# Performance work log

Measured on AMD Instinct MI355X. Metric: run time of the kernel, lower is better.

The kernel has to match this reference:

```python
import jax, jax.numpy as jnp
import numpy as np

HIDDEN = 128
GRID = 8
NB = 32.0            # neighborhood_size
CELL = NB / GRID      # cell_size


def setup_inputs() -> dict:
    key = jax.random.key(0)
    k1, k2, k3, k4 = jax.random.split(key, 4)
    N = 1024
    hidden_states = jax.random.normal(k1, (N, HIDDEN), dtype=jnp.float32)
    positions = jax.random.uniform(k2, (N, 2), dtype=jnp.float32) * 100.0
    fan_in = GRID * GRID * HIDDEN
    bound = 1.0 / np.sqrt(fan_in)
    W = jax.random.uniform(k3, (fan_in, HIDDEN), dtype=jnp.float32, minval=-bound, maxval=bound)
    b = jax.random.uniform(k4, (HIDDEN,), dtype=jnp.float32, minval=-bound, maxval=bound)
    return {"hidden_states": hidden_states, "positions": positions, "W": W, "b": b}


def reference(hidden_states, positions, W, b):
    N, H = hidden_states.shape
    G = GRID
    pos = jax.lax.stop_gradient(positions)  # indices carry no gradient (matches torch int())
    # rel[i, j] = positions[j] - positions[i]
    rel = pos[None, :, :] - pos[:, None, :]                      # [N, N, 2]
    half = NB / 2.0
    inside = (jnp.abs(rel[..., 0]) <= half) & (jnp.abs(rel[..., 1]) <= half)
    not_self = ~jnp.eye(N, dtype=bool)
    valid = inside & not_self                                     # [N, N]
    # rel + half is in [0, NB] when inside, so floor == int() truncation
    gx = jnp.clip(jnp.floor((rel[..., 0] + half) / CELL).astype(jnp.int32), 0, G - 1)
    gy = jnp.clip(jnp.floor((rel[..., 1] + half) / CELL).astype(jnp.int32), 0, G - 1)
    cell = gy * G + gx                                            # [N, N], in [0, G*G)
    # invalid pairs go to a dummy cell G*G per pedestrian
    seg = jnp.where(valid, cell, G * G)
    gid = (jnp.arange(N, dtype=jnp.int32)[:, None] * (G * G + 1) + seg).reshape(-1)
    data = jnp.broadcast_to(hidden_states[None, :, :], (N, N, H)).reshape(N * N, H)
    gmax = jax.ops.segment_max(data, gid, num_segments=N * (G * G + 1))  # [N*(G*G+1), H]
    # torch grid starts at zeros and uses maximum -> clamp at 0; empty cells (-inf) -> 0
    grid = jnp.maximum(gmax.reshape(N, G * G + 1, H)[:, : G * G, :], 0.0)  # [N, G*G, H]
    flat = grid.reshape(N, G * G * H)
    return flat @ W + b
```

## Files before the change

### kernel.cpp

```cpp
#include <hip/hip_runtime.h>
#include <hip/hip_bf16.h>

#define N_PED 1024
#define H 128
#define G 8
#define NCELL 64
#define K_TOT 8192
#define HALF_NB 16.0f
#define INV_CELL 0.25f

#define KSPLIT 16
#define KC 512
#define BM 32
#define BK 64
#define NSTAGE 8

typedef __attribute__((ext_vector_type(8))) short bf16x8;
typedef __attribute__((ext_vector_type(4))) float f32x4;

__device__ __forceinline__ unsigned map_f2u(float v) {
    unsigned u = __float_as_uint(v);
    return (u & 0x80000000u) ? ~u : (u | 0x80000000u);
}
__device__ __forceinline__ float unmap_u2f(unsigned u) {
    return __uint_as_float((u & 0x80000000u) ? (u ^ 0x80000000u) : ~u);
}
__device__ __forceinline__ ushort f2bf(float f) {
    unsigned u = __float_as_uint(f);
    return (ushort)((u + 0x7FFFu + ((u >> 16) & 1u)) >> 16);
}
__device__ __forceinline__ void gl_lds16(const void* g, void* l) {
    __builtin_amdgcn_global_load_lds(
        (const __attribute__((address_space(1))) void*)g,
        (__attribute__((address_space(3))) void*)l, 16, 0, 0);
}

__global__ __launch_bounds__(512) void fused_pre(const float* __restrict__ hs,
                                                 const float* __restrict__ pos,
                                                 const float* __restrict__ W,
                                                 ushort* __restrict__ grid,
                                                 ushort* __restrict__ Wt) {
    __shared__ __align__(16) char smem[36872];
    const int tid = threadIdx.x;

    if (blockIdx.x < N_PED) {
        unsigned* lgrid = (unsigned*)smem;
        int*      list  = (int*)(smem + 32768);
        int*      cnt   = (int*)(smem + 36864);
        const int i = blockIdx.x;

        const unsigned iu = 0x80000000u;
        uint4 iv = {iu, iu, iu, iu};
        for (int k = tid; k < NCELL * H / 4; k += 512) ((uint4*)lgrid)[k] = iv;
        if (tid == 0) *cnt = 0;
        __syncthreads();

        const float2 pi = ((const float2*)pos)[i];
        for (int j = tid; j < N_PED; j += 512) {
            float2 pj = ((const float2*)pos)[j];
            float rx = pj.x - pi.x;
            float ry = pj.y - pi.y;
            if (j != i && fabsf(rx) <= HALF_NB && fabsf(ry) <= HALF_NB) {
                int gx = (int)floorf((rx + HALF_NB) * INV_CELL);
                int gy = (int)floorf((ry + HALF_NB) * INV_CELL);
                gx = min(G - 1, max(0, gx));
                gy = min(G - 1, max(0, gy));
                int slot = atomicAdd(cnt, 1);
                list[slot] = (j << 8) | (gy * G + gx);
            }
        }
        __syncthreads();

        const int n    = *cnt;
        const int dim4 = (tid & 31) * 4;
        const int eg   = tid >> 5;
        int e  = eg;
        int p0 = (e < n) ? list[e] : -1;
        int p1 = (e + 16 < n) ? list[e + 16] : -1;
        float4 v0 = {};
        if (p0 >= 0) v0 = *(const float4*)&hs[(p0 >> 8) * H + dim4];
        while (p0 >= 0) {
            int p2 = (e + 32 < n) ? list[e + 32] : -1;
            float4 v1 = {};
            if (p1 >= 0) v1 = *(const float4*)&hs[(p1 >> 8) * H + dim4];
            unsigned* gph = &lgrid[(p0 & 255) * H + dim4];
            atomicMax(gph + 0, map_f2u(v0.x));
            atomicMax(gph + 1, map_f2u(v0.y));
            atomicMax(gph + 2, map_f2u(v0.z));
            atomicMax(gph + 3, map_f2u(v0.w));
            e += 16; p0 = p1; p1 = p2; v0 = v1;
        }
        __syncthreads();

        ushort* dst = grid + (size_t)i * K_TOT;
        for (int c = tid; c < K_TOT / 8; c += 512) {
            uint4 a = ((const uint4*)lgrid)[2 * c];
            uint4 b = ((const uint4*)lgrid)[2 * c + 1];
            ushort tmp[8];
            tmp[0] = f2bf(unmap_u2f(a.x)); tmp[1] = f2bf(unmap_u2f(a.y));
            tmp[2] = f2bf(unmap_u2f(a.z)); tmp[3] = f2bf(unmap_u2f(a.w));
            tmp[4] = f2bf(unmap_u2f(b.x)); tmp[5] = f2bf(unmap_u2f(b.y));
            tmp[6] = f2bf(unmap_u2f(b.z)); tmp[7] = f2bf(unmap_u2f(b.w));
            *(bf16x8*)&dst[8 * c] = *(const bf16x8*)tmp;
        }
    } else {
        float* tile = (float*)smem;
        const int bw  = blockIdx.x - N_PED;
        const int k0w = bw * 64;

        for (int x = tid; x < 64 * H; x += 512) {
            int r = x >> 7, c = x & 127;
            tile[r * 129 + c] = W[(size_t)(k0w + r) * H + c];
        }
        __syncthreads();

        const int col = tid >> 2;
        const int kh  = (tid & 3) * 16;
        ushort tmp[16];
        #pragma unroll
        for (int t = 0; t < 16; ++t) tmp[t] = f2bf(tile[(kh + t) * 129 + col]);
        ushort* w0 = Wt + (size_t)col * K_TOT + k0w + kh;
        *(bf16x8*)w0       = *(const bf16x8*)&tmp[0];
        *(bf16x8*)(w0 + 8) = *(const bf16x8*)&tmp[8];
    }
}

__global__ __launch_bounds__(256) void gemm_mfma(const ushort* __restrict__ A,
                                                 const ushort* __restrict__ Wt,
                                                 float* __restrict__ part) {
    __shared__ ushort sA[3][BM * BK];
    __shared__ ushort sB[3][H * BK];

    const int m0   = blockIdx.x * BM;
    const int k0   = blockIdx.y * KC;
    const int tid  = threadIdx.x;
    const int wave = tid >> 6;
    const int lane = tid & 63;
    const int ll   = lane & 15;
    const int lh   = lane >> 4;
    const int lr8  = lane >> 3;
    const int cswz = (lane & 7) ^ (lr8 & 7);

    const ushort* Abase = A  + (size_t)(m0 + 8 * wave + lr8) * K_TOT + k0 + cswz * 8;
    const ushort* Bbase = Wt + (size_t)(32 * wave + lr8) * K_TOT      + k0 + cswz * 8;

    f32x4 acc[2][2] = {};

#define STAGE(T, BUF)                                                        \
    do {                                                                     \
        gl_lds16(Abase + (T) * BK, &sA[BUF][8 * wave * BK]);                 \
        gl_lds16(Bbase + (T) * BK,                &sB[BUF][(32 * wave) * BK]);      \
        gl_lds16(Bbase + (T) * BK +  8 * K_TOT,   &sB[BUF][(32 * wave + 8) * BK]);  \
        gl_lds16(Bbase + (T) * BK + 16 * K_TOT,   &sB[BUF][(32 * wave + 16) * BK]); \
        gl_lds16(Bbase + (T) * BK + 24 * K_TOT,   &sB[BUF][(32 * wave + 24) * BK]); \
    } while (0)

    STAGE(0, 0);
    STAGE(1, 1);
    asm volatile("s_waitcnt vmcnt(5)" ::: "memory");
    __builtin_amdgcn_s_barrier();

    #pragma unroll
    for (int t = 0; t < NSTAGE; ++t) {
        if (t + 2 < NSTAGE) STAGE(t + 2, (t + 2) % 3);

        const int buf = t % 3;
        #pragma unroll
        for (int ks = 0; ks < 2; ++ks) {
            const int chunk = ks * 4 + lh;
            bf16x8 bfrag[2], afrag[2];
            #pragma unroll
            for (int nt = 0; nt < 2; ++nt) {
                int br = wave * 32 + nt * 16 + ll;
                bfrag[nt] = *(const bf16x8*)&sB[buf][br * BK + ((chunk ^ (br & 7)) * 8)];
            }
            #pragma unroll
            for (int mt = 0; mt < 2; ++mt) {
                int ar = mt * 16 + ll;
                afrag[mt] = *(const bf16x8*)&sA[buf][ar * BK + ((chunk ^ (ar & 7)) * 8)];
            }
            #pragma unroll
            for (int mt = 0; mt < 2; ++mt)
                #pragma unroll
                for (int nt = 0; nt < 2; ++nt)
                    acc[mt][nt] = __builtin_amdgcn_mfma_f32_16x16x32_bf16(
                        afrag[mt], bfrag[nt], acc[mt][nt], 0, 0, 0);
        }

        if (t + 1 < NSTAGE) {
            if (t + 2 < NSTAGE)
                asm volatile("s_waitcnt vmcnt(5)" ::: "memory");
            else
                asm volatile("s_waitcnt vmcnt(0)" ::: "memory");
            __builtin_amdgcn_s_barrier();
        }
    }
#undef STAGE

    float* dst = part + (size_t)blockIdx.y * (N_PED * H);
    #pragma unroll
    for (int mt = 0; mt < 2; ++mt)
        #pragma unroll
        for (int nt = 0; nt < 2; ++nt) {
            int col   = wave * 32 + nt * 16 + ll;
            int rbase = m0 + mt * 16 + lh * 4;
            #pragma unroll
            for (int r = 0; r < 4; ++r)
                dst[(size_t)(rbase + r) * H + col] = acc[mt][nt][r];
        }
}

__global__ __launch_bounds__(128) void reduce_out(const float* __restrict__ part,
                                                  const float* __restrict__ b,
                                                  float* __restrict__ out) {
    const int idx = (blockIdx.x * 128 + threadIdx.x) * 4;
    float4 acc = *(const float4*)&b[idx & (H - 1)];
    #pragma unroll
    for (int s = 0; s < KSPLIT; ++s) {
        float4 p = *(const float4*)&part[(size_t)s * (N_PED * H) + idx];
        acc.x += p.x; acc.y += p.y; acc.z += p.z; acc.w += p.w;
    }
    *(float4*)&out[idx] = acc;
}

extern "C" void kernel_launch(void* const* d_in, const int* in_sizes, int n_in,
                              void* d_out, int out_size, void* d_ws, size_t ws_size,
                              hipStream_t stream) {
    const float* hs  = (const float*)d_in[0];
    const float* pos = (const float*)d_in[1];
    const float* Wm  = (const float*)d_in[2];
    const float* b   = (const float*)d_in[3];
    float* out = (float*)d_out;

    ushort* grid = (ushort*)d_ws;
    ushort* Wt   = (ushort*)((char*)d_ws + (16u << 20));
    float*  part = (float*)((char*)d_ws + (18u << 20));

    fused_pre<<<N_PED + K_TOT / 64, 512, 0, stream>>>(hs, pos, Wm, grid, Wt);
    gemm_mfma<<<dim3(N_PED / BM, KSPLIT), 256, 0, stream>>>(grid, Wt, part);
    reduce_out<<<(N_PED * H) / (128 * 4), 128, 0, stream>>>(part, b, out);
}
```

Measured before the change: 30.17 us.

## Replace split-K partial buffer and reduce kernel with atomic accumulation into output

The preprocessing kernel now also initializes the output with the broadcast bias using two extra blocks. The GEMM drops LDS staging and loads fragments directly from global memory into MFMA operands, then atomically adds its split-K partial results straight into the output. This removes the partial-sum buffer round trip and the third kernel launch. In exchange it adds float atomics, which contend and make summation order nondeterministic, and issues uncoalesced direct global loads with no software pipelining.

```diff
diff --git a/kernel.cpp b/kernel.cpp
--- a/kernel.cpp
+++ b/kernel.cpp
@@ -11,9 +11,6 @@
 
 #define KSPLIT 16
 #define KC 512
-#define BM 32
-#define BK 64
-#define NSTAGE 8
 
 typedef __attribute__((ext_vector_type(8))) short bf16x8;
 typedef __attribute__((ext_vector_type(4))) float f32x4;
@@ -29,17 +26,14 @@
     unsigned u = __float_as_uint(f);
     return (ushort)((u + 0x7FFFu + ((u >> 16) & 1u)) >> 16);
 }
-__device__ __forceinline__ void gl_lds16(const void* g, void* l) {
-    __builtin_amdgcn_global_load_lds(
-        (const __attribute__((address_space(1))) void*)g,
-        (__attribute__((address_space(3))) void*)l, 16, 0, 0);
-}
 
 __global__ __launch_bounds__(512) void fused_pre(const float* __restrict__ hs,
                                                  const float* __restrict__ pos,
                                                  const float* __restrict__ W,
+                                                 const float* __restrict__ b,
                                                  ushort* __restrict__ grid,
-                                                 ushort* __restrict__ Wt) {
+                                                 ushort* __restrict__ Wt,
+                                                 float* __restrict__ out) {
     __shared__ __align__(16) char smem[36872];
     const int tid = threadIdx.x;
 
@@ -61,10 +55,8 @@
             float rx = pj.x - pi.x;
             float ry = pj.y - pi.y;
             if (j != i && fabsf(rx) <= HALF_NB && fabsf(ry) <= HALF_NB) {
-                int gx = (int)floorf((rx + HALF_NB) * INV_CELL);
-                int gy = (int)floorf((ry + HALF_NB) * INV_CELL);
-                gx = min(G - 1, max(0, gx));
-                gy = min(G - 1, max(0, gy));
+                int gx = min(G - 1, max(0, (int)floorf((rx + HALF_NB) * INV_CELL)));
+                int gy = min(G - 1, max(0, (int)floorf((ry + HALF_NB) * INV_CELL)));
                 int slot = atomicAdd(cnt, 1);
                 list[slot] = (j << 8) | (gy * G + gx);
             }
@@ -95,15 +87,15 @@
         ushort* dst = grid + (size_t)i * K_TOT;
         for (int c = tid; c < K_TOT / 8; c += 512) {
             uint4 a = ((const uint4*)lgrid)[2 * c];
-            uint4 b = ((const uint4*)lgrid)[2 * c + 1];
+            uint4 bq = ((const uint4*)lgrid)[2 * c + 1];
             ushort tmp[8];
-            tmp[0] = f2bf(unmap_u2f(a.x)); tmp[1] = f2bf(unmap_u2f(a.y));
-            tmp[2] = f2bf(unmap_u2f(a.z)); tmp[3] = f2bf(unmap_u2f(a.w));
-            tmp[4] = f2bf(unmap_u2f(b.x)); tmp[5] = f2bf(unmap_u2f(b.y));
-            tmp[6] = f2bf(unmap_u2f(b.z)); tmp[7] = f2bf(unmap_u2f(b.w));
+            tmp[0] = f2bf(unmap_u2f(a.x));  tmp[1] = f2bf(unmap_u2f(a.y));
+            tmp[2] = f2bf(unmap_u2f(a.z));  tmp[3] = f2bf(unmap_u2f(a.w));
+            tmp[4] = f2bf(unmap_u2f(bq.x)); tmp[5] = f2bf(unmap_u2f(bq.y));
+            tmp[6] = f2bf(unmap_u2f(bq.z)); tmp[7] = f2bf(unmap_u2f(bq.w));
             *(bf16x8*)&dst[8 * c] = *(const bf16x8*)tmp;
         }
-    } else {
+    } else if (blockIdx.x < N_PED + 128) {
         float* tile = (float*)smem;
         const int bw  = blockIdx.x - N_PED;
         const int k0w = bw * 64;
@@ -122,105 +114,54 @@
         ushort* w0 = Wt + (size_t)col * K_TOT + k0w + kh;
         *(bf16x8*)w0       = *(const bf16x8*)&tmp[0];
         *(bf16x8*)(w0 + 8) = *(const bf16x8*)&tmp[8];
+    } else {
+        const float4* b4 = (const float4*)b;
+        float4* out4 = (float4*)out;
+        const int b0 = (blockIdx.x - N_PED - 128) * 16384;
+        for (int i2 = tid; i2 < 16384; i2 += 512) {
+            int g = b0 + i2;
+            out4[g] = b4[g & 31];
+        }
     }
 }
 
-__global__ __launch_bounds__(256) void gemm_mfma(const ushort* __restrict__ A,
-                                                 const ushort* __restrict__ Wt,
-                                                 float* __restrict__ part) {
-    __shared__ ushort sA[3][BM * BK];
-    __shared__ ushort sB[3][H * BK];
-
-    const int m0   = blockIdx.x * BM;
+__global__ __launch_bounds__(256) void gemm_direct(const ushort* __restrict__ A,
+                                                   const ushort* __restrict__ Wt,
+                                                   float* __restrict__ out) {
+    const int m0   = blockIdx.x * 32;
     const int k0   = blockIdx.y * KC;
     const int tid  = threadIdx.x;
-    const int wave = tid >> 6;
-    const int lane = tid & 63;
-    const int ll   = lane & 15;
-    const int lh   = lane >> 4;
-    const int lr8  = lane >> 3;
-    const int cswz = (lane & 7) ^ (lr8 & 7);
+    const int wave = tid >> 6, lane = tid & 63;
+    const int ll   = lane & 15, lh = lane >> 4;
 
-    const ushort* Abase = A  + (size_t)(m0 + 8 * wave + lr8) * K_TOT + k0 + cswz * 8;
-    const ushort* Bbase = Wt + (size_t)(32 * wave + lr8) * K_TOT      + k0 + cswz * 8;
+    const ushort* Ab = A  + (size_t)(m0 + ll) * K_TOT        + k0 + lh * 8;
+    const ushort* Bb = Wt + (size_t)(wave * 32 + ll) * K_TOT + k0 + lh * 8;
 
     f32x4 acc[2][2] = {};
 
-#define STAGE(T, BUF)                                                        \
-    do {                                                                     \
-        gl_lds16(Abase + (T) * BK, &sA[BUF][8 * wave * BK]);                 \
-        gl_lds16(Bbase + (T) * BK,                &sB[BUF][(32 * wave) * BK]);      \
-        gl_lds16(Bbase + (T) * BK +  8 * K_TOT,   &sB[BUF][(32 * wave + 8) * BK]);  \
-        gl_lds16(Bbase + (T) * BK + 16 * K_TOT,   &sB[BUF][(32 * wave + 16) * BK]); \
-        gl_lds16(Bbase + (T) * BK + 24 * K_TOT,   &sB[BUF][(32 * wave + 24) * BK]); \
-    } while (0)
+    #pragma unroll 4
+    for (int ks = 0; ks < KC / 32; ++ks) {
+        const int kk = ks * 32;
+        bf16x8 a0 = *(const bf16x8*)(Ab + kk);
+        bf16x8 a1 = *(const bf16x8*)(Ab + (size_t)16 * K_TOT + kk);
+        bf16x8 b0 = *(const bf16x8*)(Bb + kk);
+        bf16x8 b1 = *(const bf16x8*)(Bb + (size_t)16 * K_TOT + kk);
+        acc[0][0] = __builtin_amdgcn_mfma_f32_16x16x32_bf16(a0, b0, acc[0][0], 0, 0, 0);
+        acc[0][1] = __builtin_amdgcn_mfma_f32_16x16x32_bf16(a0, b1, acc[0][1], 0, 0, 0);
+        acc[1][0] = __builtin_amdgcn_mfma_f32_16x16x32_bf16(a1, b0, acc[1][0], 0, 0, 0);
+        acc[1][1] = __builtin_amdgcn_mfma_f32_16x16x32_bf16(a1, b1, acc[1][1], 0, 0, 0);
+    }
 
-    STAGE(0, 0);
-    STAGE(1, 1);
-    asm volatile("s_waitcnt vmcnt(5)" ::: "memory");
-    __builtin_amdgcn_s_barrier();
-
-    #pragma unroll
-    for (int t = 0; t < NSTAGE; ++t) {
-        if (t + 2 < NSTAGE) STAGE(t + 2, (t + 2) % 3);
-
-        const int buf = t % 3;
-        #pragma unroll
-        for (int ks = 0; ks < 2; ++ks) {
-            const int chunk = ks * 4 + lh;
-            bf16x8 bfrag[2], afrag[2];
-            #pragma unroll
-            for (int nt = 0; nt < 2; ++nt) {
-                int br = wave * 32 + nt * 16 + ll;
-                bfrag[nt] = *(const bf16x8*)&sB[buf][br * BK + ((chunk ^ (br & 7)) * 8)];
-            }
-            #pragma unroll
-            for (int mt = 0; mt < 2; ++mt) {
-                int ar = mt * 16 + ll;
-                afrag[mt] = *(const bf16x8*)&sA[buf][ar * BK + ((chunk ^ (ar & 7)) * 8)];
-            }
-            #pragma unroll
-            for (int mt = 0; mt < 2; ++mt)
-                #pragma unroll
-                for (int nt = 0; nt < 2; ++nt)
-                    acc[mt][nt] = __builtin_amdgcn_mfma_f32_16x16x32_bf16(
-                        afrag[mt], bfrag[nt], acc[mt][nt], 0, 0, 0);
-        }
-
-        if (t + 1 < NSTAGE) {
-            if (t + 2 < NSTAGE)
-                asm volatile("s_waitcnt vmcnt(5)" ::: "memory");
-            else
-                asm volatile("s_waitcnt vmcnt(0)" ::: "memory");
-            __builtin_amdgcn_s_barrier();
-        }
-    }
-#undef STAGE
-
-    float* dst = part + (size_t)blockIdx.y * (N_PED * H);
     #pragma unroll
     for (int mt = 0; mt < 2; ++mt)
         #pragma unroll
         for (int nt = 0; nt < 2; ++nt) {
-            int col   = wave * 32 + nt * 16 + ll;
-            int rbase = m0 + mt * 16 + lh * 4;
+            int col = wave * 32 + nt * 16 + ll;
+            int row = m0 + mt * 16 + lh * 4;
             #pragma unroll
             for (int r = 0; r < 4; ++r)
-                dst[(size_t)(rbase + r) * H + col] = acc[mt][nt][r];
+                atomicAdd(&out[(size_t)(row + r) * H + col], acc[mt][nt][r]);
         }
-}
-
-__global__ __launch_bounds__(128) void reduce_out(const float* __restrict__ part,
-                                                  const float* __restrict__ b,
-                                                  float* __restrict__ out) {
-    const int idx = (blockIdx.x * 128 + threadIdx.x) * 4;
-    float4 acc = *(const float4*)&b[idx & (H - 1)];
-    #pragma unroll
-    for (int s = 0; s < KSPLIT; ++s) {
-        float4 p = *(const float4*)&part[(size_t)s * (N_PED * H) + idx];
-        acc.x += p.x; acc.y += p.y; acc.z += p.z; acc.w += p.w;
-    }
-    *(float4*)&out[idx] = acc;
 }
 
 extern "C" void kernel_launch(void* const* d_in, const int* in_sizes, int n_in,
@@ -234,9 +175,7 @@
 
     ushort* grid = (ushort*)d_ws;
     ushort* Wt   = (ushort*)((char*)d_ws + (16u << 20));
-    float*  part = (float*)((char*)d_ws + (18u << 20));
 
-    fused_pre<<<N_PED + K_TOT / 64, 512, 0, stream>>>(hs, pos, Wm, grid, Wt);
-    gemm_mfma<<<dim3(N_PED / BM, KSPLIT), 256, 0, stream>>>(grid, Wt, part);
-    reduce_out<<<(N_PED * H) / (128 * 4), 128, 0, stream>>>(part, b, out);
+    fused_pre<<<N_PED + 128 + 2, 512, 0, stream>>>(hs, pos, Wm, b, grid, Wt, out);
+    gemm_direct<<<dim3(N_PED / 32, KSPLIT), 256, 0, stream>>>(grid, Wt, out);
 }
```

After: 40.65 us. 34.7% more time.
